# Kernel tuning notes

Measured on AMD Instinct MI355X. Metric: run time of the kernel, lower is better.

The kernel has to match this reference:

```python
import jax, jax.numpy as jnp
import numpy as np

N_NODES = 50000
N_EDGES = 800000
IN_DIM = 128
OUT_DIM = 128
NEG_SLOPE = 0.01  # F.leaky_relu default


def setup_inputs() -> dict:
    key = jax.random.key(0)
    k_h, k_src, k_dst, k_w, k_as, k_ad = jax.random.split(key, 6)
    h = jax.random.normal(k_h, (N_NODES, IN_DIM), dtype=jnp.float32)
    src = jax.random.randint(k_src, (N_EDGES,), 0, N_NODES, dtype=jnp.int32)
    dst = jax.random.randint(k_dst, (N_EDGES,), 0, N_NODES, dtype=jnp.int32)
    # fc weight: xavier_normal with relu gain; stored as [in, out] for h @ W
    gain = float(np.sqrt(2.0))
    std_w = gain * np.sqrt(2.0 / (IN_DIM + OUT_DIM))
    W = jax.random.normal(k_w, (IN_DIM, OUT_DIM), dtype=jnp.float32) * std_w
    # attn weight [1, 2*out] split into src/dst halves (concat@a == z_s@a_s + z_d@a_d)
    std_a = gain * np.sqrt(2.0 / (2 * OUT_DIM + 1))
    a_src = jax.random.normal(k_as, (OUT_DIM,), dtype=jnp.float32) * std_a
    a_dst = jax.random.normal(k_ad, (OUT_DIM,), dtype=jnp.float32) * std_a
    return {"h": h, "src": src, "dst": dst, "W": W, "a_src": a_src, "a_dst": a_dst}


def reference(h, src, dst, W, a_src, a_dst):
    n = h.shape[0]
    z = h @ W                                   # [N, D]
    # edge attention: leaky_relu(attn(concat[z_src, z_dst]))
    e = z[src] @ a_src + z[dst] @ a_dst         # [E]
    e = jnp.where(e >= 0, e, NEG_SLOPE * e)
    # segment softmax over incoming edges of each dst node
    m = jax.ops.segment_max(e, dst, num_segments=n)    # [N]
    m = jnp.where(jnp.isfinite(m), m, 0.0)             # guard zero-in-degree nodes
    ex = jnp.exp(e - m[dst])                            # [E]
    denom = jax.ops.segment_sum(ex, dst, num_segments=n)
    denom = jnp.where(denom > 0, denom, 1.0)
    alpha = ex / denom[dst]                             # [E]
    # weighted scatter-sum of source features
    out = jax.ops.segment_sum(alpha[:, None] * z[src], dst, num_segments=n)  # [N, D]
    return out
```

## Files before the change

### kernel.cpp

```cpp
#include <hip/hip_runtime.h>
#include <math.h>

#define DIM 128
#define NEG_SLOPE 0.01f
#define CAP 64

typedef __attribute__((ext_vector_type(8))) short bf16x8;
typedef __attribute__((ext_vector_type(4))) float f32x4;
typedef unsigned int uint;
typedef unsigned short ushort;

static __device__ __forceinline__ uint f2bf(float x) {
  uint u = __float_as_uint(x);
  return (u + 0x7fffu + ((u >> 16) & 1u)) >> 16;
}

__global__ __launch_bounds__(256) void prep_fill(
    const float* __restrict__ W,
    const float* __restrict__ a_src, const float* __restrict__ a_dst,
    const float* __restrict__ h,
    const int* __restrict__ src, const int* __restrict__ dst,
    ushort* __restrict__ Wt16, float* __restrict__ s, float* __restrict__ d,
    int* __restrict__ cur, ushort* __restrict__ bucket,
    int n, int E, int nsd)
{
  __shared__ float vec[2][DIM];
  const int t = threadIdx.x;
  const int b = blockIdx.x;

  if (b == 0) {
    const float4* W4 = (const float4*)W;
    #pragma unroll
    for (int it = 0; it < 16; ++it) {
      int i = t + it * 256;
      int k = i >> 5, n4 = (i & 31) * 4;
      float4 v = W4[i];
      Wt16[(n4 + 0) * 128 + k] = (ushort)f2bf(v.x);
      Wt16[(n4 + 1) * 128 + k] = (ushort)f2bf(v.y);
      Wt16[(n4 + 2) * 128 + k] = (ushort)f2bf(v.z);
      Wt16[(n4 + 3) * 128 + k] = (ushort)f2bf(v.w);
    }
  } else if (b <= nsd) {
    {
      const float* row = W + (size_t)(t & 127) * DIM;
      const float* a = (t < 128) ? a_src : a_dst;
      float acc = 0.f;
      #pragma unroll 16
      for (int j = 0; j < DIM; ++j) acc = fmaf(row[j], a[j], acc);
      vec[t >> 7][t & 127] = acc;
    }
    __syncthreads();
    int i = (b - 1) * 256 + t;
    if (i < n) {
      const float4* h4 = (const float4*)(h + (size_t)i * DIM);
      float sp = 0.f, dp = 0.f;
      #pragma unroll 8
      for (int c = 0; c < 32; ++c) {
        float4 v = h4[c];
        sp = fmaf(v.x, vec[0][c*4+0], fmaf(v.y, vec[0][c*4+1],
             fmaf(v.z, vec[0][c*4+2], fmaf(v.w, vec[0][c*4+3], sp))));
        dp = fmaf(v.x, vec[1][c*4+0], fmaf(v.y, vec[1][c*4+1],
             fmaf(v.z, vec[1][c*4+2], fmaf(v.w, vec[1][c*4+3], dp))));
      }
      s[i] = sp; d[i] = dp;
    }
  } else {
    int i = (b - 1 - nsd) * 256 + t;
    if (i < E) {
      int sj = src[i], dj = dst[i];
      int c = atomicAdd(&cur[dj], 1);
      if (c < CAP)
        bucket[dj * CAP + c] = (ushort)sj;
    }
  }
}

__global__ __launch_bounds__(256) void gemm_mfma(
    const float* __restrict__ h, const ushort* __restrict__ Wt16,
    uint* __restrict__ zb,
    int n)
{
  __shared__ __align__(16) ushort hb[64 * 136];
  __shared__ __align__(16) ushort Wt[128 * 136];

  const int t = threadIdx.x;
  const int lane = t & 63, wv = t >> 6;
  const int row0 = blockIdx.x * 64;

  {
    const float4* h4 = (const float4*)h;
    #pragma unroll
    for (int it = 0; it < 8; ++it) {
      int i = t + it * 256;
      int r = i >> 5, c4 = i & 31;
      float4 v = make_float4(0.f, 0.f, 0.f, 0.f);
      if (row0 + r < n) v = h4[(size_t)(row0 + r) * 32 + c4];
      uint2 pk;
      pk.x = f2bf(v.x) | (f2bf(v.y) << 16);
      pk.y = f2bf(v.z) | (f2bf(v.w) << 16);
      *(uint2*)&hb[r * 136 + c4 * 4] = pk;
    }
  }
  {
    const uint4* Wg = (const uint4*)Wt16;
    #pragma unroll
    for (int it = 0; it < 8; ++it) {
      int i = t + it * 256;
      int nn = i >> 4, k8 = (i & 15) * 8;
      *(uint4*)&Wt[nn * 136 + k8] = Wg[i];
    }
  }
  __syncthreads();

  f32x4 acc[8];
  #pragma unroll
  for (int c = 0; c < 8; ++c) acc[c] = (f32x4){0.f, 0.f, 0.f, 0.f};

  const int m = lane & 15, quad = lane >> 4;
  const ushort* arow = &hb[(wv * 16 + m) * 136 + quad * 8];
  const ushort* brow = &Wt[m * 136 + quad * 8];

  #pragma unroll
  for (int ks = 0; ks < 4; ++ks) {
    bf16x8 af = *(const bf16x8*)(arow + ks * 32);
    #pragma unroll
    for (int c = 0; c < 8; ++c) {
      bf16x8 bf = *(const bf16x8*)(brow + c * 16 * 136 + ks * 32);
      acc[c] = __builtin_amdgcn_mfma_f32_16x16x32_bf16(af, bf, acc[c], 0, 0, 0);
    }
  }

  __syncthreads();
  #pragma unroll
  for (int c = 0; c < 8; ++c) {
    int col = c * 16 + m;
    #pragma unroll
    for (int reg = 0; reg < 4; ++reg) {
      int r = wv * 16 + quad * 4 + reg;
      hb[r * 136 + col] = (ushort)f2bf(acc[c][reg]);
    }
  }
  __syncthreads();
  #pragma unroll
  for (int it = 0; it < 4; ++it) {
    int i = t + it * 256;
    int r = i >> 4, c8 = i & 15;
    int rg = row0 + r;
    if (rg < n) {
      uint4 v = *(uint4*)&hb[r * 136 + c8 * 8];
      *(uint4*)&zb[(size_t)rg * 64 + c8 * 4] = v;
    }
  }
}

__global__ __launch_bounds__(256) void gat_node(
    const uint* __restrict__ zb, const float* __restrict__ s,
    const float* __restrict__ d, const int* __restrict__ cur,
    const ushort* __restrict__ bucket, float* __restrict__ out, int n)
{
  int wave = threadIdx.x >> 6;
  int lane = threadIdx.x & 63;
  int node = blockIdx.x * 4 + wave;
  if (node >= n) return;

  int cnt = min(cur[node], CAP);
  float2* out2 = (float2*)out;
  if (cnt <= 0) {
    out2[(size_t)node * 64 + lane] = make_float2(0.f, 0.f);
    return;
  }

  float dn = d[node];
  int sj = 0; float w = 0.f;
  if (lane < cnt) {
    sj = (int)bucket[node * CAP + lane];
    float e = s[sj] + dn;
    e = (e >= 0.f) ? e : NEG_SLOPE * e;
    w = __expf(e);
  }
  float denom = w;
  #pragma unroll
  for (int o = 32; o > 0; o >>= 1) denom += __shfl_xor(denom, o, 64);

  float2 acc = make_float2(0.f, 0.f);
  int tt = 0;
  for (; tt + 8 <= cnt; tt += 8) {
    uint zv[8]; float wt[8];
    #pragma unroll
    for (int u = 0; u < 8; ++u) {
      int st = __shfl(sj, tt + u, 64);
      zv[u] = zb[(size_t)st * 64 + lane];
      wt[u] = __shfl(w, tt + u, 64);
    }
    #pragma unroll
    for (int u = 0; u < 8; ++u) {
      acc.x = fmaf(wt[u], __uint_as_float(zv[u] << 16), acc.x);
      acc.y = fmaf(wt[u], __uint_as_float(zv[u] & 0xffff0000u), acc.y);
    }
  }
  for (; tt < cnt; ++tt) {
    int st = __shfl(sj, tt, 64);
    uint u = zb[(size_t)st * 64 + lane];
    float wt = __shfl(w, tt, 64);
    acc.x = fmaf(wt, __uint_as_float(u << 16), acc.x);
    acc.y = fmaf(wt, __uint_as_float(u & 0xffff0000u), acc.y);
  }
  float inv = 1.f / denom;
  out2[(size_t)node * 64 + lane] = make_float2(acc.x * inv, acc.y * inv);
}

extern "C" void kernel_launch(void* const* d_in, const int* in_sizes, int n_in,
                              void* d_out, int out_size, void* d_ws, size_t ws_size,
                              hipStream_t stream)
{
  const float* h     = (const float*)d_in[0];
  const int*   src   = (const int*)d_in[1];
  const int*   dst   = (const int*)d_in[2];
  const float* W     = (const float*)d_in[3];
  const float* a_src = (const float*)d_in[4];
  const float* a_dst = (const float*)d_in[5];
  float* out = (float*)d_out;

  const int n = in_sizes[0] / DIM;
  const int E = in_sizes[1];

  char* ws = (char*)d_ws;
  uint* zb       = (uint*)ws;   ws += (size_t)n * 64 * 4;
  float* s       = (float*)ws;  ws += (size_t)n * 4;
  float* d       = (float*)ws;  ws += (size_t)n * 4;
  int* cur       = (int*)ws;    ws += (size_t)n * 4;
  ushort* Wt16   = (ushort*)ws; ws += (size_t)DIM * DIM * 2;
  ushort* bucket = (ushort*)ws;

  const int nsd   = (n + 255) / 256;
  const int nfill = (E + 255) / 256;
  const int ngemm = (n + 63) / 64;

  hipMemsetAsync(cur, 0, (size_t)n * 4, stream);
  prep_fill<<<1 + nsd + nfill, 256, 0, stream>>>(
      W, a_src, a_dst, h, src, dst, Wt16, s, d, cur, bucket, n, E, nsd);
  gemm_mfma<<<ngemm, 256, 0, stream>>>(h, Wt16, zb, n);
  gat_node<<<(n + 3) / 4, 256, 0, stream>>>(zb, s, d, cur, bucket, out, n);
}
```

Before: 171.4 us.

## Fuse edge bucketing, score dots and GEMM into one kernel; zero counters in-kernel

Replaces the memset plus the prep_fill and gemm_mfma launches with a small init kernel and one fused kernel. The init kernel builds the bf16 transposed W and zeroes the per-node counters. The fused kernel splits blocks by role: edge bucketing at four edges per thread, per-node score dot products, and the MFMA GEMM, so the independent phases run side by side. The GEMM now reads its B fragments straight from global Wt16 instead of staging them in LDS. This cuts LDS use per block and allows higher occupancy, but brings uncoalesced global B loads into the MFMA inner loop.

```diff
diff --git a/kernel.cpp b/kernel.cpp
--- a/kernel.cpp
+++ b/kernel.cpp
@@ -15,19 +15,11 @@
   return (u + 0x7fffu + ((u >> 16) & 1u)) >> 16;
 }
 
-__global__ __launch_bounds__(256) void prep_fill(
-    const float* __restrict__ W,
-    const float* __restrict__ a_src, const float* __restrict__ a_dst,
-    const float* __restrict__ h,
-    const int* __restrict__ src, const int* __restrict__ dst,
-    ushort* __restrict__ Wt16, float* __restrict__ s, float* __restrict__ d,
-    int* __restrict__ cur, ushort* __restrict__ bucket,
-    int n, int E, int nsd)
-{
-  __shared__ float vec[2][DIM];
-  const int t = threadIdx.x;
-  const int b = blockIdx.x;
-
+__global__ __launch_bounds__(256) void init_k(
+    const float* __restrict__ W, ushort* __restrict__ Wt16,
+    int* __restrict__ cur, int n)
+{
+  const int t = threadIdx.x, b = blockIdx.x;
   if (b == 0) {
     const float4* W4 = (const float4*)W;
     #pragma unroll
@@ -40,52 +32,78 @@
       Wt16[(n4 + 2) * 128 + k] = (ushort)f2bf(v.z);
       Wt16[(n4 + 3) * 128 + k] = (ushort)f2bf(v.w);
     }
-  } else if (b <= nsd) {
+  } else {
+    int i = (b - 1) * 256 + t;
+    if (i < n) cur[i] = 0;
+  }
+}
+
+__global__ __launch_bounds__(256, 4) void mega(
+    const float* __restrict__ W,
+    const float* __restrict__ a_src, const float* __restrict__ a_dst,
+    const float* __restrict__ h,
+    const int* __restrict__ src, const int* __restrict__ dst,
+    const ushort* __restrict__ Wt16,
+    float* __restrict__ s, float* __restrict__ d,
+    int* __restrict__ cur, ushort* __restrict__ bucket,
+    uint* __restrict__ zb,
+    int n, int E, int nfill, int nsd)
+{
+  __shared__ __align__(16) ushort smem[64 * 136];
+  const int t = threadIdx.x;
+  const int b = blockIdx.x;
+
+  if (b < nfill) {
+    int base = b * 1024 + t;
+    int sj[4], dj[4], c[4];
+    #pragma unroll
+    for (int u = 0; u < 4; ++u) {
+      int i = base + u * 256;
+      dj[u] = -1;
+      if (i < E) { sj[u] = src[i]; dj[u] = dst[i]; }
+    }
+    #pragma unroll
+    for (int u = 0; u < 4; ++u)
+      if (dj[u] >= 0) c[u] = atomicAdd(&cur[dj[u]], 1);
+    #pragma unroll
+    for (int u = 0; u < 4; ++u)
+      if (dj[u] >= 0 && c[u] < CAP)
+        bucket[dj[u] * CAP + c[u]] = (ushort)sj[u];
+    return;
+  }
+
+  if (b < nfill + nsd) {
+    float* vec = (float*)smem;
     {
       const float* row = W + (size_t)(t & 127) * DIM;
       const float* a = (t < 128) ? a_src : a_dst;
       float acc = 0.f;
       #pragma unroll 16
       for (int j = 0; j < DIM; ++j) acc = fmaf(row[j], a[j], acc);
-      vec[t >> 7][t & 127] = acc;
+      vec[(t >> 7) * DIM + (t & 127)] = acc;
     }
     __syncthreads();
-    int i = (b - 1) * 256 + t;
+    int i = (b - nfill) * 256 + t;
     if (i < n) {
       const float4* h4 = (const float4*)(h + (size_t)i * DIM);
       float sp = 0.f, dp = 0.f;
       #pragma unroll 8
-      for (int c = 0; c < 32; ++c) {
-        float4 v = h4[c];
-        sp = fmaf(v.x, vec[0][c*4+0], fmaf(v.y, vec[0][c*4+1],
-             fmaf(v.z, vec[0][c*4+2], fmaf(v.w, vec[0][c*4+3], sp))));
-        dp = fmaf(v.x, vec[1][c*4+0], fmaf(v.y, vec[1][c*4+1],
-             fmaf(v.z, vec[1][c*4+2], fmaf(v.w, vec[1][c*4+3], dp))));
+      for (int c2 = 0; c2 < 32; ++c2) {
+        float4 v = h4[c2];
+        sp = fmaf(v.x, vec[c2*4+0], fmaf(v.y, vec[c2*4+1],
+             fmaf(v.z, vec[c2*4+2], fmaf(v.w, vec[c2*4+3], sp))));
+        dp = fmaf(v.x, vec[DIM+c2*4+0], fmaf(v.y, vec[DIM+c2*4+1],
+             fmaf(v.z, vec[DIM+c2*4+2], fmaf(v.w, vec[DIM+c2*4+3], dp))));
       }
       s[i] = sp; d[i] = dp;
     }
-  } else {
-    int i = (b - 1 - nsd) * 256 + t;
-    if (i < E) {
-      int sj = src[i], dj = dst[i];
-      int c = atomicAdd(&cur[dj], 1);
-      if (c < CAP)
-        bucket[dj * CAP + c] = (ushort)sj;
-    }
-  }
-}
-
-__global__ __launch_bounds__(256) void gemm_mfma(
-    const float* __restrict__ h, const ushort* __restrict__ Wt16,
-    uint* __restrict__ zb,
-    int n)
-{
-  __shared__ __align__(16) ushort hb[64 * 136];
-  __shared__ __align__(16) ushort Wt[128 * 136];
-
-  const int t = threadIdx.x;
+    return;
+  }
+
+  const int g = b - nfill - nsd;
   const int lane = t & 63, wv = t >> 6;
-  const int row0 = blockIdx.x * 64;
+  const int row0 = g * 64;
+  ushort* hb = smem;
 
   {
     const float4* h4 = (const float4*)h;
@@ -101,43 +119,34 @@
       *(uint2*)&hb[r * 136 + c4 * 4] = pk;
     }
   }
-  {
-    const uint4* Wg = (const uint4*)Wt16;
-    #pragma unroll
-    for (int it = 0; it < 8; ++it) {
-      int i = t + it * 256;
-      int nn = i >> 4, k8 = (i & 15) * 8;
-      *(uint4*)&Wt[nn * 136 + k8] = Wg[i];
-    }
-  }
   __syncthreads();
 
   f32x4 acc[8];
   #pragma unroll
-  for (int c = 0; c < 8; ++c) acc[c] = (f32x4){0.f, 0.f, 0.f, 0.f};
+  for (int c2 = 0; c2 < 8; ++c2) acc[c2] = (f32x4){0.f, 0.f, 0.f, 0.f};
 
   const int m = lane & 15, quad = lane >> 4;
   const ushort* arow = &hb[(wv * 16 + m) * 136 + quad * 8];
-  const ushort* brow = &Wt[m * 136 + quad * 8];
+  const ushort* bb = Wt16 + (size_t)m * 128 + quad * 8;
 
   #pragma unroll
   for (int ks = 0; ks < 4; ++ks) {
     bf16x8 af = *(const bf16x8*)(arow + ks * 32);
     #pragma unroll
-    for (int c = 0; c < 8; ++c) {
-      bf16x8 bf = *(const bf16x8*)(brow + c * 16 * 136 + ks * 32);
-      acc[c] = __builtin_amdgcn_mfma_f32_16x16x32_bf16(af, bf, acc[c], 0, 0, 0);
+    for (int c2 = 0; c2 < 8; ++c2) {
+      bf16x8 bf = *(const bf16x8*)(bb + c2 * 2048 + ks * 32);
+      acc[c2] = __builtin_amdgcn_mfma_f32_16x16x32_bf16(af, bf, acc[c2], 0, 0, 0);
     }
   }
 
   __syncthreads();
   #pragma unroll
-  for (int c = 0; c < 8; ++c) {
-    int col = c * 16 + m;
+  for (int c2 = 0; c2 < 8; ++c2) {
+    int col = c2 * 16 + m;
     #pragma unroll
     for (int reg = 0; reg < 4; ++reg) {
       int r = wv * 16 + quad * 4 + reg;
-      hb[r * 136 + col] = (ushort)f2bf(acc[c][reg]);
+      hb[r * 136 + col] = (ushort)f2bf(acc[c2][reg]);
     }
   }
   __syncthreads();
@@ -233,12 +242,13 @@
   ushort* bucket = (ushort*)ws;
 
   const int nsd   = (n + 255) / 256;
-  const int nfill = (E + 255) / 256;
+  const int nfill = (E + 1023) / 1024;
   const int ngemm = (n + 63) / 64;
-
-  hipMemsetAsync(cur, 0, (size_t)n * 4, stream);
-  prep_fill<<<1 + nsd + nfill, 256, 0, stream>>>(
-      W, a_src, a_dst, h, src, dst, Wt16, s, d, cur, bucket, n, E, nsd);
-  gemm_mfma<<<ngemm, 256, 0, stream>>>(h, Wt16, zb, n);
+  const int nzero = (n + 255) / 256;
+
+  init_k<<<1 + nzero, 256, 0, stream>>>(W, Wt16, cur, n);
+  mega<<<nfill + nsd + ngemm, 256, 0, stream>>>(
+      W, a_src, a_dst, h, src, dst, Wt16, s, d, cur, bucket, zb,
+      n, E, nfill, nsd);
   gat_node<<<(n + 3) / 4, 256, 0, stream>>>(zb, s, d, cur, bucket, out, n);
 }
```

After: 186.6 us. 1.09x slower.

## Partition edge bucketing by destination slice and replace memset with init kernel

Applied to the files above, without the earlier changes.

The edge bucketing is restructured so that each chunk of 8192 edges is read by 8 blocks. Each block handles only the destinations in its eighth of the node range, so the atomics and bucket writes of a block stay within a narrow address range, which should improve locality and cache behaviour. The edge arrays are read as vectorised nontemporal loads, with a scalar tail loop. The hipMemsetAsync is replaced by a small init kernel that zeroes the counters and also does the W transpose. The cost is reading src and dst eight times over and adding one more kernel launch.

```diff
diff --git a/kernel.cpp b/kernel.cpp
--- a/kernel.cpp
+++ b/kernel.cpp
@@ -4,9 +4,11 @@
 #define DIM 128
 #define NEG_SLOPE 0.01f
 #define CAP 64
+#define EPB 8192
 
 typedef __attribute__((ext_vector_type(8))) short bf16x8;
 typedef __attribute__((ext_vector_type(4))) float f32x4;
+typedef __attribute__((ext_vector_type(4))) int i32x4;
 typedef unsigned int uint;
 typedef unsigned short ushort;
 
@@ -15,19 +17,11 @@
   return (u + 0x7fffu + ((u >> 16) & 1u)) >> 16;
 }
 
-__global__ __launch_bounds__(256) void prep_fill(
-    const float* __restrict__ W,
-    const float* __restrict__ a_src, const float* __restrict__ a_dst,
-    const float* __restrict__ h,
-    const int* __restrict__ src, const int* __restrict__ dst,
-    ushort* __restrict__ Wt16, float* __restrict__ s, float* __restrict__ d,
-    int* __restrict__ cur, ushort* __restrict__ bucket,
-    int n, int E, int nsd)
-{
-  __shared__ float vec[2][DIM];
-  const int t = threadIdx.x;
-  const int b = blockIdx.x;
-
+__global__ __launch_bounds__(256) void init_k(
+    const float* __restrict__ W, ushort* __restrict__ Wt16,
+    int* __restrict__ cur, int n)
+{
+  const int t = threadIdx.x, b = blockIdx.x;
   if (b == 0) {
     const float4* W4 = (const float4*)W;
     #pragma unroll
@@ -40,7 +34,26 @@
       Wt16[(n4 + 2) * 128 + k] = (ushort)f2bf(v.z);
       Wt16[(n4 + 3) * 128 + k] = (ushort)f2bf(v.w);
     }
-  } else if (b <= nsd) {
+  } else {
+    int i = (b - 1) * 256 + t;
+    if (i < n) cur[i] = 0;
+  }
+}
+
+__global__ __launch_bounds__(256) void prep_fill(
+    const float* __restrict__ W,
+    const float* __restrict__ a_src, const float* __restrict__ a_dst,
+    const float* __restrict__ h,
+    const int* __restrict__ src, const int* __restrict__ dst,
+    float* __restrict__ s, float* __restrict__ d,
+    int* __restrict__ cur, ushort* __restrict__ bucket,
+    int n, int E, int nsd, int spp)
+{
+  __shared__ float vec[2][DIM];
+  const int t = threadIdx.x;
+  const int b = blockIdx.x;
+
+  if (b < nsd) {
     {
       const float* row = W + (size_t)(t & 127) * DIM;
       const float* a = (t < 128) ? a_src : a_dst;
@@ -50,7 +63,7 @@
       vec[t >> 7][t & 127] = acc;
     }
     __syncthreads();
-    int i = (b - 1) * 256 + t;
+    int i = b * 256 + t;
     if (i < n) {
       const float4* h4 = (const float4*)(h + (size_t)i * DIM);
       float sp = 0.f, dp = 0.f;
@@ -64,13 +77,40 @@
       }
       s[i] = sp; d[i] = dp;
     }
-  } else {
-    int i = (b - 1 - nsd) * 256 + t;
-    if (i < E) {
-      int sj = src[i], dj = dst[i];
-      int c = atomicAdd(&cur[dj], 1);
-      if (c < CAP)
-        bucket[dj * CAP + c] = (ushort)sj;
+    return;
+  }
+
+  const int slice = b & 7;
+  const int chunk = (b - nsd) >> 3;
+  const int lo = slice * spp;
+  const int hi = min(n, lo + spp);
+  const i32x4* s4 = (const i32x4*)src;
+  const i32x4* d4 = (const i32x4*)dst;
+  const int base4 = chunk * (EPB / 4);
+
+  #pragma unroll
+  for (int it = 0; it < EPB / 4 / 256; ++it) {
+    int i4 = base4 + it * 256 + t;
+    int i = i4 * 4;
+    if (i + 3 < E) {
+      i32x4 dv = __builtin_nontemporal_load(&d4[i4]);
+      i32x4 sv = __builtin_nontemporal_load(&s4[i4]);
+      #pragma unroll
+      for (int u = 0; u < 4; ++u) {
+        int dj = dv[u];
+        if (dj >= lo && dj < hi) {
+          int c = atomicAdd(&cur[dj], 1);
+          if (c < CAP) bucket[dj * CAP + c] = (ushort)sv[u];
+        }
+      }
+    } else if (i < E) {
+      for (int e = i; e < E; ++e) {
+        int dj = dst[e];
+        if (dj >= lo && dj < hi) {
+          int c = atomicAdd(&cur[dj], 1);
+          if (c < CAP) bucket[dj * CAP + c] = (ushort)src[e];
+        }
+      }
     }
   }
 }
@@ -232,13 +272,15 @@
   ushort* Wt16   = (ushort*)ws; ws += (size_t)DIM * DIM * 2;
   ushort* bucket = (ushort*)ws;
 
-  const int nsd   = (n + 255) / 256;
-  const int nfill = (E + 255) / 256;
-  const int ngemm = (n + 63) / 64;
-
-  hipMemsetAsync(cur, 0, (size_t)n * 4, stream);
-  prep_fill<<<1 + nsd + nfill, 256, 0, stream>>>(
-      W, a_src, a_dst, h, src, dst, Wt16, s, d, cur, bucket, n, E, nsd);
+  const int nsd    = (n + 255) / 256;
+  const int nchunk = (E + EPB - 1) / EPB;
+  const int ngemm  = (n + 63) / 64;
+  const int nzero  = (n + 255) / 256;
+  const int spp    = (n + 7) / 8;
+
+  init_k<<<1 + nzero, 256, 0, stream>>>(W, Wt16, cur, n);
+  prep_fill<<<nsd + 8 * nchunk, 256, 0, stream>>>(
+      W, a_src, a_dst, h, src, dst, s, d, cur, bucket, n, E, nsd, spp);
   gemm_mfma<<<ngemm, 256, 0, stream>>>(h, Wt16, zb, n);
   gat_node<<<(n + 3) / 4, 256, 0, stream>>>(zb, s, d, cur, bucket, out, n);
 }
```

Result: slower. 182.5 us (+6.5%).
